# Kernel optimization log

Measured on AMD Instinct MI355X. Metric: run time of the kernel, lower is better.

Reference implementation:

```python
import jax, jax.numpy as jnp
import numpy as np

NEG_INF = -1000.0
EPS = 1e-5

M, B, D = 1024, 8, 1024
H = 16
DH = D // H
FF = 4096


def _layer_norm(x, g, b):
    mu = jnp.mean(x, axis=-1, keepdims=True)
    var = jnp.mean((x - mu) ** 2, axis=-1, keepdims=True)
    return (x - mu) * jax.lax.rsqrt(var + EPS) * g + b


def setup_inputs() -> dict:
    key = jax.random.key(0)
    ks = jax.random.split(key, 12)
    s = 0.02
    return {
        "x": jax.random.normal(ks[0], (M, B, D), jnp.float32),
        "src_mask": jnp.zeros((M, B), jnp.bool_),
        "ln1_g": jnp.ones((D,), jnp.float32),
        "ln1_b": jnp.zeros((D,), jnp.float32),
        "wq": jax.random.normal(ks[1], (D, D), jnp.float32) * s,
        "bq": jnp.zeros((D,), jnp.float32),
        "wk": jax.random.normal(ks[2], (D, D), jnp.float32) * s,
        "bk": jnp.zeros((D,), jnp.float32),
        "wv": jax.random.normal(ks[3], (D, D), jnp.float32) * s,
        "bv": jnp.zeros((D,), jnp.float32),
        "wo": jax.random.normal(ks[4], (D, D), jnp.float32) * s,
        "bo": jnp.zeros((D,), jnp.float32),
        "ln2_g": jnp.ones((D,), jnp.float32),
        "ln2_b": jnp.zeros((D,), jnp.float32),
        "w1": jax.random.normal(ks[5], (D, FF), jnp.float32) * s,
        "b1": jnp.zeros((FF,), jnp.float32),
        "w2": jax.random.normal(ks[6], (FF, D), jnp.float32) * s,
        "b2": jnp.zeros((D,), jnp.float32),
    }


def reference(x, src_mask, ln1_g, ln1_b, wq, bq, wk, bk, wv, bv, wo, bo,
              ln2_g, ln2_b, w1, b1, w2, b2):
    m, bsz, d = x.shape
    # --- self-attention sublayer ---
    xn = _layer_norm(x, ln1_g, ln1_b)
    q = (xn @ wq + bq).reshape(m, bsz, H, DH)
    k = (xn @ wk + bk).reshape(m, bsz, H, DH)
    v = (xn @ wv + bv).reshape(m, bsz, H, DH)
    # NOTE: original has NO 1/sqrt(head_dim) scaling
    potentials = jnp.einsum('mbhi,nbhj->mnbh', q, k)  # [m,n,b,h]
    potentials = jnp.where(src_mask[None, :, :, None], NEG_INF, potentials)
    weights = jax.nn.softmax(potentials, axis=1)
    pooled = jnp.einsum('mnbh,nbhi->mbhi', weights, v).reshape(m, bsz, d)
    att = pooled @ wo + bo
    x = x + att
    # --- feed-forward sublayer ---
    xn = _layer_norm(x, ln2_g, ln2_b)
    h = jax.nn.relu(xn @ w1 + b1)
    return h @ w2 + b2 + x
```

## Files before the change

### kernel.cpp

```cpp
#include <hip/hip_runtime.h>
#include <hip/hip_bf16.h>

typedef float fv4 __attribute__((ext_vector_type(4)));
typedef __bf16 bfv8 __attribute__((ext_vector_type(8)));
typedef unsigned short u16;

#define DEV static __device__ __forceinline__

DEV u16 f2bf(float f) {
  union { __hip_bfloat16 h; u16 u; } c;
  c.h = __float2bfloat16(f);
  return c.u;
}

DEV void glds16(const void* g, void* l) {
  __builtin_amdgcn_global_load_lds(
      (const __attribute__((address_space(1))) unsigned int*)g,
      (__attribute__((address_space(3))) unsigned int*)l, 16, 0, 0);
}

DEV fv4 mfma16(bfv8 a, bfv8 b, fv4 c) {
  return __builtin_amdgcn_mfma_f32_16x16x32_bf16(a, b, c, 0, 0, 0);
}

template <bool OUT_BF16, bool RELU, bool RESID, bool BIAS>
__global__ __launch_bounds__(256, 2) void gemm_k(
    const u16* __restrict__ A, const u16* __restrict__ Bt,
    const float* __restrict__ bias, const float* __restrict__ resid,
    void* __restrict__ outp, int K, int N, int lda, int ldb) {
  __shared__ __align__(16) u16 lds[2][2][128 * 32];
  const int tid = threadIdx.x;
  const int lane = tid & 63, wid = tid >> 6;
  const int bm0 = blockIdx.y * 128, bn0 = blockIdx.x * 128;
  const int wr = (wid >> 1) * 64, wc = (wid & 1) * 64;
  const int g = lane >> 4, ml = lane & 15;

  fv4 acc[4][4];
#pragma unroll
  for (int i = 0; i < 4; ++i)
#pragma unroll
    for (int j = 0; j < 4; ++j) acc[i][j] = (fv4)0.f;

  const int nK = K >> 5;

  auto stage = [&](int t) {
    const int buf = t & 1;
    const int k0 = t * 32;
#pragma unroll
    for (int p = 0; p < 2; ++p) {
      const int s = p * 256 + tid;
      const int r0 = ((s >> 2) & 1) ^ ((s >> 4) & 1);
      const int row = ((s >> 3) << 1) | r0;
      const int chunk = (s & 3) ^ (row & 3);
      glds16(A + (size_t)(bm0 + row) * lda + k0 + chunk * 8,
             &lds[buf][0][(p * 256 + wid * 64) * 8]);
      glds16(Bt + (size_t)(bn0 + row) * ldb + k0 + chunk * 8,
             &lds[buf][1][(p * 256 + wid * 64) * 8]);
    }
  };

  stage(0);
  for (int t = 0; t < nK; ++t) {
    __syncthreads();
    if (t + 1 < nK) stage(t + 1);
    const u16* Ab = lds[t & 1][0];
    const u16* Bb = lds[t & 1][1];
    bfv8 af[4], bf[4];
#pragma unroll
    for (int f = 0; f < 4; ++f) {
      const int ra = wr + f * 16 + ml;
      const int ba = ((ra << 6) + (g << 4)) ^ ((ra & 7) << 4);
      af[f] = *(const bfv8*)&Ab[ba >> 1];
      const int rb = wc + f * 16 + ml;
      const int bb = ((rb << 6) + (g << 4)) ^ ((rb & 7) << 4);
      bf[f] = *(const bfv8*)&Bb[bb >> 1];
    }
#pragma unroll
    for (int i = 0; i < 4; ++i)
#pragma unroll
      for (int j = 0; j < 4; ++j) acc[i][j] = mfma16(af[i], bf[j], acc[i][j]);
  }

#pragma unroll
  for (int j = 0; j < 4; ++j) {
    const int n = bn0 + wc + j * 16 + ml;
    float bv = 0.f;
    if (BIAS) bv = bias[n];
#pragma unroll
    for (int i = 0; i < 4; ++i) {
      const int m0r = bm0 + wr + i * 16 + g * 4;
#pragma unroll
      for (int r = 0; r < 4; ++r) {
        float val = acc[i][j][r] + bv;
        if (RESID) val += resid[(size_t)(m0r + r) * N + n];
        if (RELU) val = fmaxf(val, 0.f);
        if (OUT_BF16)
          ((u16*)outp)[(size_t)(m0r + r) * N + n] = f2bf(val);
        else
          ((float*)outp)[(size_t)(m0r + r) * N + n] = val;
      }
    }
  }
}

__global__ __launch_bounds__(256, 2) void attn2_k(
    const u16* __restrict__ v, const float* __restrict__ qsarr,
    const float* __restrict__ ksarr, const unsigned char* __restrict__ mask,
    u16* __restrict__ pooled) {
  __shared__ float ks_s[1024];
  __shared__ float red[16];
  __shared__ int anym_s;
  __shared__ float zl[4][16];
  __shared__ __align__(16) u16 VT[64 * 72];

  const int tid = threadIdx.x, lane = tid & 63, wid = tid >> 6;
  const int g = lane >> 4, ml = lane & 15;
  const int b = blockIdx.y >> 4, h = blockIdx.y & 15;
  const int m0 = blockIdx.x * 64;

  if (tid == 0) anym_s = 0;
  __syncthreads();

  const float* ksp = ksarr + (size_t)(b * 16 + h) * 1024;
  float4 kv = *(const float4*)&ksp[tid * 4];
  *(float4*)&ks_s[tid * 4] = kv;
  const float kvv[4] = {kv.x, kv.y, kv.z, kv.w};
  float mx = -3.4e38f, mn = 3.4e38f;
  int am = 0;
#pragma unroll
  for (int j = 0; j < 4; ++j) {
    const int n = tid * 4 + j;
    const int mk = mask[(size_t)n * 8 + b] ? 1 : 0;
    am |= mk;
    if (!mk) { mx = fmaxf(mx, kvv[j]); mn = fminf(mn, kvv[j]); }
  }
  if (am) atomicOr(&anym_s, 1);
#pragma unroll
  for (int s = 1; s <= 32; s <<= 1) {
    mx = fmaxf(mx, __shfl_xor(mx, s, 64));
    mn = fminf(mn, __shfl_xor(mn, s, 64));
  }
  if (lane == 0) { red[wid] = mx; red[8 + wid] = mn; }
  __syncthreads();
  const float smax = fmaxf(fmaxf(red[0], red[1]), fmaxf(red[2], red[3]));
  const float smin = fminf(fminf(red[8], red[9]), fminf(red[10], red[11]));
  const int anym = anym_s;

  const float c = qsarr[(size_t)(b * 16 + h) * 1024 + m0 + wid * 16 + ml];
  const float M = (c >= 0.f) ? c * smax : c * smin;

  fv4 o[4];
#pragma unroll
  for (int d = 0; d < 4; ++d) o[d] = (fv4)0.f;
  float zacc = 0.f;

  for (int nt = 0; nt < 16; ++nt) {
    const int n0 = nt * 64;
    if (nt) __syncthreads();
#pragma unroll
    for (int p = 0; p < 2; ++p) {
      const int s = p * 256 + tid;
      const int n = s >> 3, cc = s & 7;
      bfv8 vv = *(const bfv8*)&v[((size_t)(n0 + n) * 8 + b) * 1024 + h * 64 + cc * 8];
      const u16* vb = (const u16*)&vv;
#pragma unroll
      for (int j = 0; j < 8; ++j) VT[(cc * 8 + j) * 72 + n] = vb[j];
    }
    __syncthreads();

    bfv8 pa[2];
#pragma unroll
    for (int kk = 0; kk < 2; ++kk) {
      const int kb = n0 + kk * 32 + g * 8;
      const float4 s0 = *(const float4*)&ks_s[kb - n0 + n0];
      const float4 s1 = *(const float4*)&ks_s[kb + 4];
      const float sv[8] = {s0.x, s0.y, s0.z, s0.w, s1.x, s1.y, s1.z, s1.w};
      u16 tmp[8];
#pragma unroll
      for (int j = 0; j < 8; ++j) {
        float p = __expf(fmaf(c, sv[j], -M));
        if (anym && mask[(size_t)(kb + j) * 8 + b]) p = 0.f;
        zacc += p;
        tmp[j] = f2bf(p);
      }
      pa[kk] = *(const bfv8*)tmp;
    }
#pragma unroll
    for (int kk = 0; kk < 2; ++kk)
#pragma unroll
      for (int ds = 0; ds < 4; ++ds) {
        bfv8 vf = *(const bfv8*)&VT[(ds * 16 + ml) * 72 + kk * 32 + g * 8];
        o[ds] = mfma16(pa[kk], vf, o[ds]);
      }
  }

  zacc += __shfl_xor(zacc, 16, 64);
  zacc += __shfl_xor(zacc, 32, 64);
  if (g == 0) zl[wid][ml] = zacc;
  asm volatile("" ::: "memory");
  float zin[4];
#pragma unroll
  for (int r = 0; r < 4; ++r) zin[r] = 1.f / zl[wid][g * 4 + r];

  __syncthreads();
  u16* stg = &VT[wid * 16 * 72];
#pragma unroll
  for (int ds = 0; ds < 4; ++ds)
#pragma unroll
    for (int r = 0; r < 4; ++r)
      stg[(g * 4 + r) * 72 + ds * 16 + ml] = f2bf(o[ds][r] * zin[r]);
  asm volatile("" ::: "memory");
#pragma unroll
  for (int p = 0; p < 2; ++p) {
    const int ch = p * 64 + lane;
    const int mr = ch >> 3, cc = ch & 7;
    bfv8 val = *(const bfv8*)&stg[mr * 72 + cc * 8];
    *(bfv8*)&pooled[((size_t)(m0 + wid * 16 + mr) * 8 + b) * 1024 + h * 64 + cc * 8] = val;
  }
}

__global__ __launch_bounds__(256) void ln_k(
    const float* __restrict__ x, const float* __restrict__ gw,
    const float* __restrict__ bw, u16* __restrict__ out) {
  __shared__ float sm[8];
  const int row = blockIdx.x, tid = threadIdx.x;
  const int lane = tid & 63, wid = tid >> 6;
  const float4 xv = *(const float4*)&x[(size_t)row * 1024 + tid * 4];
  float s = xv.x + xv.y + xv.z + xv.w;
  float q = xv.x * xv.x + xv.y * xv.y + xv.z * xv.z + xv.w * xv.w;
#pragma unroll
  for (int m = 1; m <= 32; m <<= 1) {
    s += __shfl_xor(s, m, 64);
    q += __shfl_xor(q, m, 64);
  }
  if (lane == 0) { sm[wid] = s; sm[4 + wid] = q; }
  __syncthreads();
  s = sm[0] + sm[1] + sm[2] + sm[3];
  q = sm[4] + sm[5] + sm[6] + sm[7];
  const float mean = s * (1.f / 1024.f);
  const float var = q * (1.f / 1024.f) - mean * mean;
  const float rstd = rsqrtf(var + 1e-5f);
  const float4 gv = *(const float4*)&gw[tid * 4];
  const float4 bv = *(const float4*)&bw[tid * 4];
  ushort4 ov;
  ov.x = f2bf((xv.x - mean) * rstd * gv.x + bv.x);
  ov.y = f2bf((xv.y - mean) * rstd * gv.y + bv.y);
  ov.z = f2bf((xv.z - mean) * rstd * gv.z + bv.z);
  ov.w = f2bf((xv.w - mean) * rstd * gv.w + bv.w);
  *(ushort4*)&out[(size_t)row * 1024 + tid * 4] = ov;
}

__global__ __launch_bounds__(256) void qks2_k(
    const float* __restrict__ x, const float* __restrict__ A,
    const float* __restrict__ S12, float* __restrict__ qsarr,
    float* __restrict__ ksarr) {
  __shared__ __align__(16) float Alds[128 * 36];
  __shared__ float wred[4][8][2][32];
  __shared__ float wred2[4][8][2][2];
  __shared__ float rowstat[16][2];

  const int t = threadIdx.x;
  const int rowp = t & 7, sub = t >> 3;
  const int wid = t >> 6, lane = t & 63;
  const int r0 = blockIdx.x * 16;

  float acc[2][32];
#pragma unroll
  for (int rr = 0; rr < 2; ++rr)
#pragma unroll
    for (int i = 0; i < 32; ++i) acc[rr][i] = 0.f;
  float sx[2] = {0.f, 0.f}, sq[2] = {0.f, 0.f};

  for (int ch = 0; ch < 8; ++ch) {
    __syncthreads();
#pragma unroll
    for (int j = 0; j < 4; ++j) {
      const int f = t + 256 * j;
      const float4 av = *(const float4*)&A[ch * 4096 + f * 4];
      *(float4*)&Alds[(f >> 3) * 36 + (f & 7) * 4] = av;
    }
    __syncthreads();
#pragma unroll
    for (int rr = 0; rr < 2; ++rr) {
      const int row = r0 + rowp * 2 + rr;
      const float4 xv = *(const float4*)&x[(size_t)row * 1024 + ch * 128 + sub * 4];
      const float xs[4] = {xv.x, xv.y, xv.z, xv.w};
#pragma unroll
      for (int kk = 0; kk < 4; ++kk) {
        sx[rr] += xs[kk];
        sq[rr] = fmaf(xs[kk], xs[kk], sq[rr]);
        const float* ap = &Alds[(sub * 4 + kk) * 36];
#pragma unroll
        for (int i = 0; i < 32; ++i)
          acc[rr][i] = fmaf(xs[kk], ap[i], acc[rr][i]);
      }
    }
  }

#pragma unroll
  for (int m = 8; m <= 32; m <<= 1) {
#pragma unroll
    for (int rr = 0; rr < 2; ++rr) {
      sx[rr] += __shfl_xor(sx[rr], m, 64);
      sq[rr] += __shfl_xor(sq[rr], m, 64);
#pragma unroll
      for (int i = 0; i < 32; ++i)
        acc[rr][i] += __shfl_xor(acc[rr][i], m, 64);
    }
  }
  if (lane < 8) {
#pragma unroll
    for (int rr = 0; rr < 2; ++rr) {
#pragma unroll
      for (int i = 0; i < 32; ++i) wred[wid][lane][rr][i] = acc[rr][i];
      wred2[wid][lane][rr][0] = sx[rr];
      wred2[wid][lane][rr][1] = sq[rr];
    }
  }
  __syncthreads();

  if (t < 16) {
    float s = 0.f, q = 0.f;
#pragma unroll
    for (int w = 0; w < 4; ++w) {
      s += wred2[w][t >> 1][t & 1][0];
      q += wred2[w][t >> 1][t & 1][1];
    }
    const float mu = s * (1.f / 1024.f);
    const float var = q * (1.f / 1024.f) - mu * mu;
    rowstat[t][0] = mu;
    rowstat[t][1] = rsqrtf(var + 1e-5f);
  }
  __syncthreads();

#pragma unroll
  for (int o = 0; o < 2; ++o) {
    const int idx = t * 2 + o;
    const int rl = idx >> 5, h = idx & 31;
    const float dot = wred[0][rl >> 1][rl & 1][h] + wred[1][rl >> 1][rl & 1][h] +
                      wred[2][rl >> 1][rl & 1][h] + wred[3][rl >> 1][rl & 1][h];
    const float mu = rowstat[rl][0], rstd = rowstat[rl][1];
    const float val = rstd * (dot - mu * S12[h]) + S12[32 + h];
    const int row = r0 + rl, mm = row >> 3, bb = row & 7;
    if (h < 16)
      qsarr[(size_t)(bb * 16 + h) * 1024 + mm] = val;
    else
      ksarr[(size_t)(bb * 16 + h - 16) * 1024 + mm] = val;
  }
}

__global__ void wsum_k(const float* __restrict__ wq,
                       const float* __restrict__ wk,
                       float* __restrict__ wqsa) {
  const int k = blockIdx.x, t = threadIdx.x;
  const int h32 = t >> 3, ch = t & 7;
  const float* src = (h32 < 16) ? (wq + (size_t)k * 1024 + h32 * 64 + ch * 8)
                                : (wk + (size_t)k * 1024 + (h32 - 16) * 64 + ch * 8);
  float s = 0.f;
#pragma unroll
  for (int j = 0; j < 8; ++j) s += src[j];
  s += __shfl_xor(s, 1, 64);
  s += __shfl_xor(s, 2, 64);
  s += __shfl_xor(s, 4, 64);
  if (ch == 0) wqsa[k * 32 + h32] = s;
}

__global__ void bsum_k(const float* __restrict__ bq,
                       const float* __restrict__ bk,
                       float* __restrict__ bqks) {
  const int t = threadIdx.x;
  if (t < 32) {
    const float* s = (t < 16) ? (bq + t * 64) : (bk + (t - 16) * 64);
    float a = 0.f;
    for (int j = 0; j < 64; ++j) a += s[j];
    bqks[t] = a;
  }
}

__global__ void afill_k(const float* __restrict__ wqsa,
                        const float* __restrict__ g,
                        float* __restrict__ A) {
  const int f = blockIdx.x * 256 + threadIdx.x;
  const float gv = g[f >> 3];
  const float4 wv = *(const float4*)&wqsa[f * 4];
  float4 av;
  av.x = wv.x * gv; av.y = wv.y * gv; av.z = wv.z * gv; av.w = wv.w * gv;
  *(float4*)&A[f * 4] = av;
}

__global__ void s12_k(const float* __restrict__ wqsa,
                      const float* __restrict__ g,
                      const float* __restrict__ lb,
                      const float* __restrict__ bqks,
                      float* __restrict__ S12) {
  __shared__ float red1[8][32], red2[8][32];
  const int t = threadIdx.x;
  const int h = t & 31, seg = t >> 5;
  float s1 = 0.f, s2 = 0.f;
  for (int k = seg * 128; k < seg * 128 + 128; ++k) {
    const float a = wqsa[k * 32 + h];
    s1 = fmaf(g[k], a, s1);
    s2 = fmaf(lb[k], a, s2);
  }
  red1[seg][h] = s1;
  red2[seg][h] = s2;
  __syncthreads();
  if (t < 32) {
    float a1 = 0.f, a2 = 0.f;
#pragma unroll
    for (int s = 0; s < 8; ++s) { a1 += red1[s][t]; a2 += red2[s][t]; }
    S12[t] = a1;
    S12[32 + t] = a2 + bqks[t];
  }
}

__global__ void tr_k(const float* __restrict__ W, u16* __restrict__ Wt,
                     int R, int C) {
  __shared__ float tile[32][33];
  const int x = threadIdx.x, y = threadIdx.y;
  const int c0 = blockIdx.x * 32, r0 = blockIdx.y * 32;
#pragma unroll
  for (int i = 0; i < 4; ++i)
    tile[y + i * 8][x] = W[(size_t)(r0 + y + i * 8) * C + c0 + x];
  __syncthreads();
#pragma unroll
  for (int i = 0; i < 4; ++i)
    Wt[(size_t)(c0 + y + i * 8) * R + r0 + x] = f2bf(tile[x][y + i * 8]);
}

extern "C" void kernel_launch(void* const* d_in, const int* in_sizes, int n_in,
                              void* d_out, int out_size, void* d_ws,
                              size_t ws_size, hipStream_t stream) {
  const float* x = (const float*)d_in[0];
  const unsigned char* mask = (const unsigned char*)d_in[1];
  const float* ln1g = (const float*)d_in[2];
  const float* ln1b = (const float*)d_in[3];
  const float* wq = (const float*)d_in[4];
  const float* bq = (const float*)d_in[5];
  const float* wk = (const float*)d_in[6];
  const float* bk = (const float*)d_in[7];
  const float* wv = (const float*)d_in[8];
  const float* bv = (const float*)d_in[9];
  const float* wo = (const float*)d_in[10];
  const float* bo = (const float*)d_in[11];
  const float* ln2g = (const float*)d_in[12];
  const float* ln2b = (const float*)d_in[13];
  const float* w1 = (const float*)d_in[14];
  const float* b1 = (const float*)d_in[15];
  const float* w2 = (const float*)d_in[16];
  const float* b2 = (const float*)d_in[17];

  u16* wvT = (u16*)d_ws;
  u16* woT = wvT + 1024 * 1024;
  u16* w1T = woT + 1024 * 1024;
  u16* w2T = w1T + 4096 * 1024;
  float* wqsa = (float*)(w2T + 1024 * 4096);
  float* bqks = wqsa + 1024 * 32;
  float* Aq = bqks + 32;
  float* S12 = Aq + 1024 * 32;
  float* qsarr = S12 + 64;
  float* ksarr = qsarr + 8 * 16 * 1024;
  u16* v = (u16*)(ksarr + 8 * 16 * 1024);
  u16* pooled = v + (size_t)8192 * 1024;
  u16* xn = pooled + (size_t)8192 * 1024;
  u16* hbuf = v;
  float* x2 = (float*)d_out;

  const dim3 b256(256), btr(32, 8);
  tr_k<<<dim3(32, 32), btr, 0, stream>>>(wv, wvT, 1024, 1024);
  tr_k<<<dim3(32, 32), btr, 0, stream>>>(wo, woT, 1024, 1024);
  tr_k<<<dim3(128, 32), btr, 0, stream>>>(w1, w1T, 1024, 4096);
  tr_k<<<dim3(32, 128), btr, 0, stream>>>(w2, w2T, 4096, 1024);
  wsum_k<<<dim3(1024), b256, 0, stream>>>(wq, wk, wqsa);
  bsum_k<<<dim3(1), dim3(64), 0, stream>>>(bq, bk, bqks);
  afill_k<<<dim3(32), b256, 0, stream>>>(wqsa, ln1g, Aq);
  s12_k<<<dim3(1), b256, 0, stream>>>(wqsa, ln1g, ln1b, bqks, S12);

  ln_k<<<dim3(8192), b256, 0, stream>>>(x, ln1g, ln1b, xn);
  qks2_k<<<dim3(512), b256, 0, stream>>>(x, Aq, S12, qsarr, ksarr);
  gemm_k<true, false, false, true><<<dim3(8, 64), b256, 0, stream>>>(
      xn, wvT, bv, nullptr, v, 1024, 1024, 1024, 1024);
  attn2_k<<<dim3(16, 128), b256, 0, stream>>>(v, qsarr, ksarr, mask, pooled);
  gemm_k<false, false, true, true><<<dim3(8, 64), b256, 0, stream>>>(
      pooled, woT, bo, x, x2, 1024, 1024, 1024, 1024);
  ln_k<<<dim3(8192), b256, 0, stream>>>(x2, ln2g, ln2b, xn);
  gemm_k<true, true, false, true><<<dim3(16, 64), b256, 0, stream>>>(
      xn, w1T, b1, nullptr, hbuf, 1024, 2048, 1024, 1024);
  gemm_k<false, false, true, true><<<dim3(8, 64), b256, 0, stream>>>(
      hbuf, w2T, b2, x2, x2, 2048, 1024, 2048, 4096);
  gemm_k<true, true, false, true><<<dim3(16, 64), b256, 0, stream>>>(
      xn, w1T + (size_t)2048 * 1024, b1 + 2048, nullptr, hbuf, 1024, 2048,
      1024, 1024);
  gemm_k<false, false, true, false><<<dim3(8, 64), b256, 0, stream>>>(
      hbuf, w2T + 2048, nullptr, x2, x2, 2048, 1024, 2048, 4096);
}
```

Baseline: 538.6 us.

## Pre-transpose V, widen attention tiles with double-buffered LDS, remap GEMM block order

```diff
diff --git a/kernel.cpp b/kernel.cpp
--- a/kernel.cpp
+++ b/kernel.cpp
@@ -31,7 +31,11 @@
   __shared__ __align__(16) u16 lds[2][2][128 * 32];
   const int tid = threadIdx.x;
   const int lane = tid & 63, wid = tid >> 6;
-  const int bm0 = blockIdx.y * 128, bn0 = blockIdx.x * 128;
+  const int gx = gridDim.x;
+  const int nwg = gx * gridDim.y;
+  int wg = blockIdx.y * gx + blockIdx.x;
+  wg = (wg & 7) * (nwg >> 3) + (wg >> 3);
+  const int bm0 = (wg / gx) * 128, bn0 = (wg % gx) * 128;
   const int wr = (wid >> 1) * 64, wc = (wid & 1) * 64;
   const int g = lane >> 4, ml = lane & 15;
 
@@ -103,25 +107,55 @@
   }
 }
 
-__global__ __launch_bounds__(256, 2) void attn2_k(
-    const u16* __restrict__ v, const float* __restrict__ qsarr,
+__global__ __launch_bounds__(256) void vt_k(const u16* __restrict__ v,
+                                            u16* __restrict__ vt) {
+  __shared__ __align__(16) u16 Tl[64 * 72];
+  const int bh = blockIdx.y, b = bh >> 4, h = bh & 15;
+  const int nt = blockIdx.x;
+  const int t = threadIdx.x;
+
+#pragma unroll
+  for (int p = 0; p < 2; ++p) {
+    const int cidx = p * 256 + t;
+    const int j = cidx >> 3, c = cidx & 7;
+    bfv8 val = *(const bfv8*)&v[((size_t)(nt * 64 + j) * 8 + b) * 1024 +
+                                h * 64 + c * 8];
+    *(bfv8*)&Tl[j * 72 + c * 8] = val;
+  }
+  __syncthreads();
+
+#pragma unroll
+  for (int p = 0; p < 2; ++p) {
+    const int cidx = p * 256 + t;
+    const int dh = cidx >> 3, nc = cidx & 7;
+    u16 tmp[8];
+#pragma unroll
+    for (int jj = 0; jj < 8; ++jj) tmp[jj] = Tl[(nc * 8 + jj) * 72 + dh];
+    *(bfv8*)&vt[((size_t)(bh * 64 + dh)) * 1024 + nt * 64 +
+                (nc ^ (dh & 7)) * 8] = *(const bfv8*)tmp;
+  }
+}
+
+__global__ __launch_bounds__(256, 2) void attn3_k(
+    const u16* __restrict__ vt, const float* __restrict__ qsarr,
     const float* __restrict__ ksarr, const unsigned char* __restrict__ mask,
     u16* __restrict__ pooled) {
   __shared__ float ks_s[1024];
   __shared__ float red[16];
   __shared__ int anym_s;
-  __shared__ float zl[4][16];
-  __shared__ __align__(16) u16 VT[64 * 72];
+  __shared__ float zl[4][4][16];
+  __shared__ __align__(16) u16 VT[2][64 * 64];
+  __shared__ __align__(16) u16 stg[4][16 * 72];
 
   const int tid = threadIdx.x, lane = tid & 63, wid = tid >> 6;
   const int g = lane >> 4, ml = lane & 15;
-  const int b = blockIdx.y >> 4, h = blockIdx.y & 15;
-  const int m0 = blockIdx.x * 64;
+  const int bh = blockIdx.y, b = bh >> 4, h = bh & 15;
+  const int mbase = blockIdx.x * 256 + wid * 64;
 
   if (tid == 0) anym_s = 0;
   __syncthreads();
 
-  const float* ksp = ksarr + (size_t)(b * 16 + h) * 1024;
+  const float* ksp = ksarr + (size_t)bh * 1024;
   float4 kv = *(const float4*)&ksp[tid * 4];
   *(float4*)&ks_s[tid * 4] = kv;
   const float kvv[4] = {kv.x, kv.y, kv.z, kv.w};
@@ -146,76 +180,105 @@
   const float smin = fminf(fminf(red[8], red[9]), fminf(red[10], red[11]));
   const int anym = anym_s;
 
-  const float c = qsarr[(size_t)(b * 16 + h) * 1024 + m0 + wid * 16 + ml];
-  const float M = (c >= 0.f) ? c * smax : c * smin;
-
-  fv4 o[4];
-#pragma unroll
-  for (int d = 0; d < 4; ++d) o[d] = (fv4)0.f;
-  float zacc = 0.f;
-
-  for (int nt = 0; nt < 16; ++nt) {
-    const int n0 = nt * 64;
-    if (nt) __syncthreads();
+  float c[4], M[4];
+#pragma unroll
+  for (int mf = 0; mf < 4; ++mf) {
+    c[mf] = qsarr[(size_t)bh * 1024 + mbase + mf * 16 + ml];
+    M[mf] = (c[mf] >= 0.f) ? c[mf] * smax : c[mf] * smin;
+  }
+
+  fv4 o[4][4];
+#pragma unroll
+  for (int mf = 0; mf < 4; ++mf)
+#pragma unroll
+    for (int d = 0; d < 4; ++d) o[mf][d] = (fv4)0.f;
+  float zacc[4] = {0.f, 0.f, 0.f, 0.f};
+
+  const size_t vtbase = (size_t)bh * 64 * 1024;
+  auto stageV = [&](int nt) {
+    const int buf = nt & 1;
 #pragma unroll
     for (int p = 0; p < 2; ++p) {
       const int s = p * 256 + tid;
-      const int n = s >> 3, cc = s & 7;
-      bfv8 vv = *(const bfv8*)&v[((size_t)(n0 + n) * 8 + b) * 1024 + h * 64 + cc * 8];
-      const u16* vb = (const u16*)&vv;
-#pragma unroll
-      for (int j = 0; j < 8; ++j) VT[(cc * 8 + j) * 72 + n] = vb[j];
-    }
+      glds16(&vt[vtbase + (size_t)(s >> 3) * 1024 + nt * 64 + (s & 7) * 8],
+             &VT[buf][s * 8]);
+    }
+  };
+
+  stageV(0);
+  for (int nt = 0; nt < 16; ++nt) {
     __syncthreads();
-
-    bfv8 pa[2];
+    if (nt + 1 < 16) stageV(nt + 1);
+    const u16* Vb = VT[nt & 1];
+    const int n0 = nt * 64;
 #pragma unroll
     for (int kk = 0; kk < 2; ++kk) {
       const int kb = n0 + kk * 32 + g * 8;
-      const float4 s0 = *(const float4*)&ks_s[kb - n0 + n0];
+      const float4 s0 = *(const float4*)&ks_s[kb];
       const float4 s1 = *(const float4*)&ks_s[kb + 4];
       const float sv[8] = {s0.x, s0.y, s0.z, s0.w, s1.x, s1.y, s1.z, s1.w};
-      u16 tmp[8];
-#pragma unroll
-      for (int j = 0; j < 8; ++j) {
-        float p = __expf(fmaf(c, sv[j], -M));
-        if (anym && mask[(size_t)(kb + j) * 8 + b]) p = 0.f;
-        zacc += p;
-        tmp[j] = f2bf(p);
+      int mk[8] = {0, 0, 0, 0, 0, 0, 0, 0};
+      if (anym) {
+#pragma unroll
+        for (int j = 0; j < 8; ++j) mk[j] = mask[(size_t)(kb + j) * 8 + b];
       }
-      pa[kk] = *(const bfv8*)tmp;
-    }
-#pragma unroll
-    for (int kk = 0; kk < 2; ++kk)
+      bfv8 pa[4];
+#pragma unroll
+      for (int mf = 0; mf < 4; ++mf) {
+        u16 tmp[8];
+#pragma unroll
+        for (int j = 0; j < 8; ++j) {
+          float p = __expf(fmaf(c[mf], sv[j], -M[mf]));
+          if (anym && mk[j]) p = 0.f;
+          zacc[mf] += p;
+          tmp[j] = f2bf(p);
+        }
+        pa[mf] = *(const bfv8*)tmp;
+      }
 #pragma unroll
       for (int ds = 0; ds < 4; ++ds) {
-        bfv8 vf = *(const bfv8*)&VT[(ds * 16 + ml) * 72 + kk * 32 + g * 8];
-        o[ds] = mfma16(pa[kk], vf, o[ds]);
+        const int d = ds * 16 + ml;
+        const int pc = (kk * 4 + g) ^ (d & 7);
+        bfv8 vf = *(const bfv8*)&Vb[d * 64 + pc * 8];
+#pragma unroll
+        for (int mf = 0; mf < 4; ++mf)
+          o[mf][ds] = mfma16(pa[mf], vf, o[mf][ds]);
       }
-  }
-
-  zacc += __shfl_xor(zacc, 16, 64);
-  zacc += __shfl_xor(zacc, 32, 64);
-  if (g == 0) zl[wid][ml] = zacc;
+    }
+  }
+
+#pragma unroll
+  for (int mf = 0; mf < 4; ++mf) {
+    zacc[mf] += __shfl_xor(zacc[mf], 16, 64);
+    zacc[mf] += __shfl_xor(zacc[mf], 32, 64);
+  }
+  if (g == 0) {
+#pragma unroll
+    for (int mf = 0; mf < 4; ++mf) zl[wid][mf][ml] = zacc[mf];
+  }
   asm volatile("" ::: "memory");
-  float zin[4];
-#pragma unroll
-  for (int r = 0; r < 4; ++r) zin[r] = 1.f / zl[wid][g * 4 + r];
-
-  __syncthreads();
-  u16* stg = &VT[wid * 16 * 72];
-#pragma unroll
-  for (int ds = 0; ds < 4; ++ds)
-#pragma unroll
-    for (int r = 0; r < 4; ++r)
-      stg[(g * 4 + r) * 72 + ds * 16 + ml] = f2bf(o[ds][r] * zin[r]);
-  asm volatile("" ::: "memory");
-#pragma unroll
-  for (int p = 0; p < 2; ++p) {
-    const int ch = p * 64 + lane;
-    const int mr = ch >> 3, cc = ch & 7;
-    bfv8 val = *(const bfv8*)&stg[mr * 72 + cc * 8];
-    *(bfv8*)&pooled[((size_t)(m0 + wid * 16 + mr) * 8 + b) * 1024 + h * 64 + cc * 8] = val;
+
+#pragma unroll
+  for (int mf = 0; mf < 4; ++mf) {
+    float zin[4];
+#pragma unroll
+    for (int r = 0; r < 4; ++r) zin[r] = 1.f / zl[wid][mf][g * 4 + r];
+#pragma unroll
+    for (int ds = 0; ds < 4; ++ds)
+#pragma unroll
+      for (int r = 0; r < 4; ++r)
+        stg[wid][(g * 4 + r) * 72 + ds * 16 + ml] =
+            f2bf(o[mf][ds][r] * zin[r]);
+    asm volatile("" ::: "memory");
+#pragma unroll
+    for (int p = 0; p < 2; ++p) {
+      const int ch = p * 64 + lane;
+      const int mr = ch >> 3, cc = ch & 7;
+      bfv8 val = *(const bfv8*)&stg[wid][mr * 72 + cc * 8];
+      *(bfv8*)&pooled[((size_t)(mbase + mf * 16 + mr) * 8 + b) * 1024 +
+                      h * 64 + cc * 8] = val;
+    }
+    asm volatile("" ::: "memory");
   }
 }
 
@@ -463,6 +526,7 @@
   u16* v = (u16*)(ksarr + 8 * 16 * 1024);
   u16* pooled = v + (size_t)8192 * 1024;
   u16* xn = pooled + (size_t)8192 * 1024;
+  u16* vtb = xn + (size_t)8192 * 1024;
   u16* hbuf = v;
   float* x2 = (float*)d_out;
 
@@ -480,7 +544,8 @@
   qks2_k<<<dim3(512), b256, 0, stream>>>(x, Aq, S12, qsarr, ksarr);
   gemm_k<true, false, false, true><<<dim3(8, 64), b256, 0, stream>>>(
       xn, wvT, bv, nullptr, v, 1024, 1024, 1024, 1024);
-  attn2_k<<<dim3(16, 128), b256, 0, stream>>>(v, qsarr, ksarr, mask, pooled);
+  vt_k<<<dim3(16, 128), b256, 0, stream>>>(v, vtb);
+  attn3_k<<<dim3(4, 128), b256, 0, stream>>>(vtb, qsarr, ksarr, mask, pooled);
   gemm_k<false, false, true, true><<<dim3(8, 64), b256, 0, stream>>>(
       pooled, woT, bo, x, x2, 1024, 1024, 1024, 1024);
   ln_k<<<dim3(8192), b256, 0, stream>>>(x2, ln2g, ln2b, xn);
```

New measurement: 477.1 us. -11.4%, faster.
